# Optimization experiments

Hardware: AMD Instinct MI355X
Metric: run time of the kernel (lower is better)

The kernel has to match this reference:

```python
import jax, jax.numpy as jnp
import numpy as np

B, HEADS, N, D, K2 = 8, 8, 3136, 32, 9

def setup_inputs() -> dict:
    key = jax.random.key(0)
    k1, k2, k3, k4, k5 = jax.random.split(key, 5)
    return {
        "q_norm": jax.random.normal(k1, (B, HEADS, N, D), dtype=jnp.float32),
        "attn_local": jax.random.normal(k2, (B, HEADS, N, K2), dtype=jnp.float32),
        "v_local": jax.random.normal(k3, (B, HEADS, N, D, K2), dtype=jnp.float32),
        "learnable_tokens": jax.random.normal(k4, (HEADS, D, K2), dtype=jnp.float32),
        "learnable_bias": jax.random.normal(k5, (HEADS, N, K2), dtype=jnp.float32),
        "window_size": 3,
        "H": 56,
        "W": 56,
    }

def reference(q_norm, attn_local, v_local, learnable_tokens, learnable_bias, window_size, H, W):
    # attn = q_norm @ learnable_tokens + learnable_bias + attn_local  -> [B,h,N,k^2]
    attn = jnp.einsum('bhnd,hdk->bhnk', q_norm, learnable_tokens) + learnable_bias + attn_local
    # out = attn @ v_local^T over the window axis -> [B,h,N,d]
    return jnp.einsum('bhnk,bhndk->bhnd', attn, v_local)
```

## Files before the change

kernel.cpp:

```cpp
#include <hip/hip_runtime.h>

constexpr int Bc   = 8;
constexpr int Hh   = 8;
constexpr int Nn   = 3136;
constexpr int Dd   = 32;
constexpr int K2c  = 9;
constexpr int ROWS = Bc * Hh * Nn;
constexpr int ROWS_PER_BLOCK = 8;
constexpr int BLOCK = 256;

__global__ __launch_bounds__(BLOCK, 4)
void swattn_av_kernel(const float* __restrict__ q,
                      const float* __restrict__ attn_local,
                      const float* __restrict__ v,
                      const float* __restrict__ tok,
                      const float* __restrict__ bias,
                      float* __restrict__ out) {
    __shared__ float T_lds[Dd * K2c];
    __shared__ float q_lds[ROWS_PER_BLOCK][Dd + 1];
    __shared__ float attn_lds[ROWS_PER_BLOCK][K2c];

    const int tid  = threadIdx.x;
    const int base = blockIdx.x * ROWS_PER_BLOCK;
    const int h    = (base / Nn) % Hh;

    T_lds[tid < Dd * K2c ? tid : 0] = tok[h * Dd * K2c + (tid < Dd * K2c ? tid : 0)];
    if (tid < Dd * K2c - BLOCK)
        T_lds[BLOCK + tid] = tok[h * Dd * K2c + BLOCK + tid];
    {
        const int lrow = tid >> 5, d = tid & 31;
        q_lds[lrow][d] = q[(base + lrow) * Dd + d];
    }
    __syncthreads();

    if (tid < ROWS_PER_BLOCK * K2c) {
        const int lrow = tid / K2c;
        const int k    = tid - lrow * K2c;
        const int gr   = base + lrow;
        float s0 = 0.f, s1 = 0.f, s2 = 0.f, s3 = 0.f;
        #pragma unroll
        for (int d = 0; d < Dd; d += 4) {
            s0 += q_lds[lrow][d + 0] * T_lds[(d + 0) * K2c + k];
            s1 += q_lds[lrow][d + 1] * T_lds[(d + 1) * K2c + k];
            s2 += q_lds[lrow][d + 2] * T_lds[(d + 2) * K2c + k];
            s3 += q_lds[lrow][d + 3] * T_lds[(d + 3) * K2c + k];
        }
        const int bn = gr % (Hh * Nn);
        attn_lds[lrow][k] = ((s0 + s1) + (s2 + s3))
                          + attn_local[gr * K2c + k]
                          + bias[bn * K2c + k];
    }
    __syncthreads();

    {
        const int lrow = tid >> 5, d = tid & 31;
        const int gr   = base + lrow;
        const float* __restrict__ vr = v + (size_t)gr * (Dd * K2c) + d * K2c;
        float acc = 0.f;
        #pragma unroll
        for (int k = 0; k < K2c; ++k)
            acc += attn_lds[lrow][k] * vr[k];
        out[gr * Dd + d] = acc;
    }
}

extern "C" void kernel_launch(void* const* d_in, const int* in_sizes, int n_in,
                              void* d_out, int out_size, void* d_ws, size_t ws_size,
                              hipStream_t stream) {
    const float* q          = (const float*)d_in[0];
    const float* attn_local = (const float*)d_in[1];
    const float* v          = (const float*)d_in[2];
    const float* tok        = (const float*)d_in[3];
    const float* bias       = (const float*)d_in[4];
    float* out = (float*)d_out;

    const int grid = ROWS / ROWS_PER_BLOCK;
    swattn_av_kernel<<<grid, BLOCK, 0, stream>>>(q, attn_local, v, tok, bias, out);
}
```

Measured before the change: 343.8 us.

## Stage v tile through LDS with coalesced float4 loads and hoist global loads

Loads the block's contiguous v slab (8 rows x 288 floats) with coalesced float4 reads into shared memory, replacing strided per-thread reads of 9 floats at stride 36 bytes. All global loads (v, tok, q, attn_local, bias) are issued up front before the first barrier so their latency overlaps. Launch bounds are raised to request more resident blocks. In exchange the kernel uses about 9 KB more LDS per block, which may limit occupancy.

Result: no change. 347.4 us (+1.0%).

```diff
diff --git a/kernel.cpp b/kernel.cpp
--- a/kernel.cpp
+++ b/kernel.cpp
@@ -6,61 +6,86 @@
 constexpr int Dd   = 32;
 constexpr int K2c  = 9;
 constexpr int ROWS = Bc * Hh * Nn;
-constexpr int ROWS_PER_BLOCK = 8;
+constexpr int RPB  = 8;
 constexpr int BLOCK = 256;
+constexpr int VROW = Dd * K2c;
+constexpr int VBLK = RPB * VROW;
 
-__global__ __launch_bounds__(BLOCK, 4)
+__global__ __launch_bounds__(BLOCK, 8)
 void swattn_av_kernel(const float* __restrict__ q,
                       const float* __restrict__ attn_local,
                       const float* __restrict__ v,
                       const float* __restrict__ tok,
                       const float* __restrict__ bias,
                       float* __restrict__ out) {
-    __shared__ float T_lds[Dd * K2c];
-    __shared__ float q_lds[ROWS_PER_BLOCK][Dd + 1];
-    __shared__ float attn_lds[ROWS_PER_BLOCK][K2c];
+    __shared__ float T_lds[VROW];
+    __shared__ float q_lds[RPB][Dd + 1];
+    __shared__ float attn_lds[RPB][K2c];
+    __shared__ float v_lds[VBLK];
 
     const int tid  = threadIdx.x;
-    const int base = blockIdx.x * ROWS_PER_BLOCK;
+    const int base = blockIdx.x * RPB;
     const int h    = (base / Nn) % Hh;
+    const int lrow = tid >> 5, d = tid & 31;
 
-    T_lds[tid < Dd * K2c ? tid : 0] = tok[h * Dd * K2c + (tid < Dd * K2c ? tid : 0)];
-    if (tid < Dd * K2c - BLOCK)
-        T_lds[BLOCK + tid] = tok[h * Dd * K2c + BLOCK + tid];
-    {
-        const int lrow = tid >> 5, d = tid & 31;
-        q_lds[lrow][d] = q[(base + lrow) * Dd + d];
+    const float4* __restrict__ vsrc =
+        reinterpret_cast<const float4*>(v + (size_t)base * VROW);
+    float4* vdst = reinterpret_cast<float4*>(v_lds);
+    float4 vv0 = vsrc[tid];
+    float4 vv1 = vsrc[tid + 256];
+    float4 vv2 = make_float4(0.f, 0.f, 0.f, 0.f);
+    if (tid < VBLK / 4 - 512)
+        vv2 = vsrc[tid + 512];
+
+    float4 tt = make_float4(0.f, 0.f, 0.f, 0.f);
+    if (tid < VROW / 4)
+        tt = reinterpret_cast<const float4*>(tok + h * VROW)[tid];
+
+    const float qv = q[(base + lrow) * Dd + d];
+
+    float al = 0.f, bs = 0.f;
+    int arow = 0, ak = 0;
+    if (tid < RPB * K2c) {
+        arow = tid / K2c;
+        ak   = tid - arow * K2c;
+        const int gr = base + arow;
+        al = attn_local[gr * K2c + ak];
+        bs = bias[(gr % (Hh * Nn)) * K2c + ak];
     }
+
+    vdst[tid]       = vv0;
+    vdst[tid + 256] = vv1;
+    if (tid < VBLK / 4 - 512)
+        vdst[tid + 512] = vv2;
+    if (tid < VROW / 4)
+        reinterpret_cast<float4*>(T_lds)[tid] = tt;
+    q_lds[lrow][d] = qv;
     __syncthreads();
 
-    if (tid < ROWS_PER_BLOCK * K2c) {
-        const int lrow = tid / K2c;
-        const int k    = tid - lrow * K2c;
-        const int gr   = base + lrow;
+    if (tid < RPB * K2c) {
         float s0 = 0.f, s1 = 0.f, s2 = 0.f, s3 = 0.f;
         #pragma unroll
-        for (int d = 0; d < Dd; d += 4) {
-            s0 += q_lds[lrow][d + 0] * T_lds[(d + 0) * K2c + k];
-            s1 += q_lds[lrow][d + 1] * T_lds[(d + 1) * K2c + k];
-            s2 += q_lds[lrow][d + 2] * T_lds[(d + 2) * K2c + k];
-            s3 += q_lds[lrow][d + 3] * T_lds[(d + 3) * K2c + k];
+        for (int dd = 0; dd < Dd; dd += 4) {
+            s0 += q_lds[arow][dd + 0] * T_lds[(dd + 0) * K2c + ak];
+            s1 += q_lds[arow][dd + 1] * T_lds[(dd + 1) * K2c + ak];
+            s2 += q_lds[arow][dd + 2] * T_lds[(dd + 2) * K2c + ak];
+            s3 += q_lds[arow][dd + 3] * T_lds[(dd + 3) * K2c + ak];
         }
-        const int bn = gr % (Hh * Nn);
-        attn_lds[lrow][k] = ((s0 + s1) + (s2 + s3))
-                          + attn_local[gr * K2c + k]
-                          + bias[bn * K2c + k];
+        attn_lds[arow][ak] = ((s0 + s1) + (s2 + s3)) + al + bs;
     }
     __syncthreads();
 
     {
-        const int lrow = tid >> 5, d = tid & 31;
-        const int gr   = base + lrow;
-        const float* __restrict__ vr = v + (size_t)gr * (Dd * K2c) + d * K2c;
+        float a[K2c];
+        #pragma unroll
+        for (int k = 0; k < K2c; ++k)
+            a[k] = attn_lds[lrow][k];
+        const float* __restrict__ vr = v_lds + lrow * VROW + d * K2c;
         float acc = 0.f;
         #pragma unroll
         for (int k = 0; k < K2c; ++k)
-            acc += attn_lds[lrow][k] * vr[k];
-        out[gr * Dd + d] = acc;
+            acc += a[k] * vr[k];
+        out[(base + lrow) * Dd + d] = acc;
     }
 }
 
@@ -74,6 +99,6 @@
     const float* bias       = (const float*)d_in[4];
     float* out = (float*)d_out;
 
-    const int grid = ROWS / ROWS_PER_BLOCK;
+    const int grid = ROWS / RPB;
     swattn_av_kernel<<<grid, BLOCK, 0, stream>>>(q, attn_local, v, tok, bias, out);
 }
```

## Use persistent waves over contiguous row runs with register double-buffered prefetch

Applied to the files above, without the earlier changes.

Replaces the one-block-per-8-rows launch with a fixed grid in which each wavefront processes a contiguous run of rows, two rows per iteration, one per 32-lane half. The next row pair's v, q and attn/bias values are prefetched into registers while the current pair is computed. The q·tokens dot product is now done with butterfly shuffles instead of shared-memory staging and block barriers. This aims to hide global load latency and remove per-block sync and launch overhead. In exchange it raises register pressure and adds many shuffles per row, since the dot product is recomputed per k.

After: 370.1 us. 1.08x slower.

```diff
diff --git a/kernel.cpp b/kernel.cpp
--- a/kernel.cpp
+++ b/kernel.cpp
@@ -6,61 +6,77 @@
 constexpr int Dd   = 32;
 constexpr int K2c  = 9;
 constexpr int ROWS = Bc * Hh * Nn;
-constexpr int ROWS_PER_BLOCK = 8;
 constexpr int BLOCK = 256;
+constexpr int WPB   = BLOCK / 64;
+constexpr int GRID  = 1792;
+constexpr int NWAVE = GRID * WPB;
+constexpr int RUN   = ROWS / NWAVE;
+constexpr int ITERS = RUN / 2;
+static_assert(NWAVE * RUN == ROWS, "exact cover");
+static_assert(Nn % RUN == 0, "run never crosses a head boundary");
+constexpr int VROW = Dd * K2c;
 
-__global__ __launch_bounds__(BLOCK, 4)
+__global__ __launch_bounds__(BLOCK, 7)
 void swattn_av_kernel(const float* __restrict__ q,
                       const float* __restrict__ attn_local,
                       const float* __restrict__ v,
                       const float* __restrict__ tok,
                       const float* __restrict__ bias,
                       float* __restrict__ out) {
-    __shared__ float T_lds[Dd * K2c];
-    __shared__ float q_lds[ROWS_PER_BLOCK][Dd + 1];
-    __shared__ float attn_lds[ROWS_PER_BLOCK][K2c];
+    __shared__ float T_lds[VROW];
 
     const int tid  = threadIdx.x;
-    const int base = blockIdx.x * ROWS_PER_BLOCK;
-    const int h    = (base / Nn) % Hh;
+    const int lane = tid & 63;
+    const int wid  = tid >> 6;
+    const int W    = blockIdx.x * WPB + wid;
+    const int runBase = W * RUN;
+    const int h    = (runBase / Nn) & (Hh - 1);
+    const int half = lane >> 5;
+    const int d    = lane & 31;
+    const bool l9  = (d < K2c);
+    const int brem = runBase % (Hh * Nn) + half;
 
-    T_lds[tid < Dd * K2c ? tid : 0] = tok[h * Dd * K2c + (tid < Dd * K2c ? tid : 0)];
-    if (tid < Dd * K2c - BLOCK)
-        T_lds[BLOCK + tid] = tok[h * Dd * K2c + BLOCK + tid];
-    {
-        const int lrow = tid >> 5, d = tid & 31;
-        q_lds[lrow][d] = q[(base + lrow) * Dd + d];
-    }
+    if (tid < VROW / 4)
+        reinterpret_cast<float4*>(T_lds)[tid] =
+            reinterpret_cast<const float4*>(tok + h * VROW)[tid];
     __syncthreads();
 
-    if (tid < ROWS_PER_BLOCK * K2c) {
-        const int lrow = tid / K2c;
-        const int k    = tid - lrow * K2c;
-        const int gr   = base + lrow;
-        float s0 = 0.f, s1 = 0.f, s2 = 0.f, s3 = 0.f;
+    float vA[K2c], vB[K2c];
+    float qA = 0.f, qB = 0.f, aA = 0.f, aB = 0.f;
+
+    auto prefetch = [&](int i, float (&vr)[K2c], float& qr, float& ar) {
+        const int r0  = runBase + 2 * i;
+        const int row = r0 + half;
+        const float* __restrict__ vp = v + (size_t)row * VROW + d * K2c;
         #pragma unroll
-        for (int d = 0; d < Dd; d += 4) {
-            s0 += q_lds[lrow][d + 0] * T_lds[(d + 0) * K2c + k];
-            s1 += q_lds[lrow][d + 1] * T_lds[(d + 1) * K2c + k];
-            s2 += q_lds[lrow][d + 2] * T_lds[(d + 2) * K2c + k];
-            s3 += q_lds[lrow][d + 3] * T_lds[(d + 3) * K2c + k];
-        }
-        const int bn = gr % (Hh * Nn);
-        attn_lds[lrow][k] = ((s0 + s1) + (s2 + s3))
-                          + attn_local[gr * K2c + k]
-                          + bias[bn * K2c + k];
-    }
-    __syncthreads();
+        for (int k = 0; k < K2c; ++k) vr[k] = vp[k];
+        qr = q[r0 * Dd + lane];
+        if (l9)
+            ar = attn_local[row * K2c + d] + bias[(brem + 2 * i) * K2c + d];
+    };
 
-    {
-        const int lrow = tid >> 5, d = tid & 31;
-        const int gr   = base + lrow;
-        const float* __restrict__ vr = v + (size_t)gr * (Dd * K2c) + d * K2c;
+    auto compute = [&](int i, float (&vr)[K2c], float qr, float ar) {
         float acc = 0.f;
         #pragma unroll
-        for (int k = 0; k < K2c; ++k)
-            acc += attn_lds[lrow][k] * vr[k];
-        out[gr * Dd + d] = acc;
+        for (int k = 0; k < K2c; ++k) {
+            float p = qr * T_lds[d * K2c + k];
+            p += __shfl_xor(p, 1, 32);
+            p += __shfl_xor(p, 2, 32);
+            p += __shfl_xor(p, 4, 32);
+            p += __shfl_xor(p, 8, 32);
+            p += __shfl_xor(p, 16, 32);
+            acc += (p + __shfl(ar, k, 32)) * vr[k];
+        }
+        out[(runBase + 2 * i) * Dd + lane] = acc;
+    };
+
+    prefetch(0, vA, qA, aA);
+    #pragma unroll
+    for (int i = 0; i < ITERS; i += 2) {
+        prefetch(i + 1, vB, qB, aB);
+        compute(i, vA, qA, aA);
+        if (i + 2 < ITERS) prefetch(i + 2, vA, qA, aA);
+        compute(i + 1, vB, qB, aB);
     }
 }
 
@@ -74,6 +90,5 @@
     const float* bias       = (const float*)d_in[4];
     float* out = (float*)d_out;
 
-    const int grid = ROWS / ROWS_PER_BLOCK;
-    swattn_av_kernel<<<grid, BLOCK, 0, stream>>>(q, attn_local, v, tok, bias, out);
+    swattn_av_kernel<<<GRID, BLOCK, 0, stream>>>(q, attn_local, v, tok, bias, out);
 }
```

## Process 32 rows per block with float4 loads and early V prefetch

Applied to the files above, without the earlier changes.

Raises rows per block from 8 to 32. Each thread now handles 4 output dims of one row, loading its 36 contiguous V floats as nine float4 registers before the attention-score phase, so the dominant V traffic overlaps the score computation. Q, tokens and the output use vectorized float4 accesses, and attn_local and bias are loaded before the first barrier. The cost is higher register pressure from the prefetched V array, and the launch bound is raised to 6 waves per SIMD.

Result: no change. 348.1 us (+1.2%).

```diff
diff --git a/kernel.cpp b/kernel.cpp
--- a/kernel.cpp
+++ b/kernel.cpp
@@ -1,66 +1,94 @@
 #include <hip/hip_runtime.h>
 
-constexpr int Bc   = 8;
 constexpr int Hh   = 8;
 constexpr int Nn   = 3136;
 constexpr int Dd   = 32;
 constexpr int K2c  = 9;
-constexpr int ROWS = Bc * Hh * Nn;
-constexpr int ROWS_PER_BLOCK = 8;
+constexpr int ROWS = 8 * Hh * Nn;
+constexpr int RPB  = 32;
 constexpr int BLOCK = 256;
+constexpr int PAIRS = RPB * K2c;
+constexpr int VROW  = Dd * K2c;
+constexpr int GRID  = ROWS / RPB;
 
-__global__ __launch_bounds__(BLOCK, 4)
+__global__ __launch_bounds__(BLOCK, 6)
 void swattn_av_kernel(const float* __restrict__ q,
                       const float* __restrict__ attn_local,
                       const float* __restrict__ v,
                       const float* __restrict__ tok,
                       const float* __restrict__ bias,
                       float* __restrict__ out) {
-    __shared__ float T_lds[Dd * K2c];
-    __shared__ float q_lds[ROWS_PER_BLOCK][Dd + 1];
-    __shared__ float attn_lds[ROWS_PER_BLOCK][K2c];
+    __shared__ float T_lds[VROW];
+    __shared__ float q_lds[RPB][Dd + 1];
+    __shared__ float attn_lds[PAIRS];
 
     const int tid  = threadIdx.x;
-    const int base = blockIdx.x * ROWS_PER_BLOCK;
-    const int h    = (base / Nn) % Hh;
+    const int base = blockIdx.x * RPB;
+    const int h    = (base / Nn) & (Hh - 1);
+    const int brem = base % (Hh * Nn);
 
-    T_lds[tid < Dd * K2c ? tid : 0] = tok[h * Dd * K2c + (tid < Dd * K2c ? tid : 0)];
-    if (tid < Dd * K2c - BLOCK)
-        T_lds[BLOCK + tid] = tok[h * Dd * K2c + BLOCK + tid];
     {
-        const int lrow = tid >> 5, d = tid & 31;
-        q_lds[lrow][d] = q[(base + lrow) * Dd + d];
+        const float4 qv = reinterpret_cast<const float4*>(q + (size_t)base * Dd)[tid];
+        const int r = tid >> 3, c = (tid & 7) * 4;
+        q_lds[r][c + 0] = qv.x;
+        q_lds[r][c + 1] = qv.y;
+        q_lds[r][c + 2] = qv.z;
+        q_lds[r][c + 3] = qv.w;
     }
+    if (tid < VROW / 4)
+        reinterpret_cast<float4*>(T_lds)[tid] =
+            reinterpret_cast<const float4*>(tok + h * VROW)[tid];
+    const float a0 = attn_local[(size_t)base * K2c + tid] + bias[(size_t)brem * K2c + tid];
+    float a1 = 0.f;
+    if (tid < PAIRS - BLOCK)
+        a1 = attn_local[(size_t)base * K2c + BLOCK + tid]
+           + bias[(size_t)brem * K2c + BLOCK + tid];
     __syncthreads();
 
-    if (tid < ROWS_PER_BLOCK * K2c) {
-        const int lrow = tid / K2c;
-        const int k    = tid - lrow * K2c;
-        const int gr   = base + lrow;
-        float s0 = 0.f, s1 = 0.f, s2 = 0.f, s3 = 0.f;
+    const int row = tid >> 3;
+    const int d0  = (tid & 7) * 4;
+    float4 vf[9];
+    {
+        const float4* __restrict__ vp = reinterpret_cast<const float4*>(
+            v + (size_t)(base + row) * VROW + d0 * K2c);
         #pragma unroll
-        for (int d = 0; d < Dd; d += 4) {
-            s0 += q_lds[lrow][d + 0] * T_lds[(d + 0) * K2c + k];
-            s1 += q_lds[lrow][d + 1] * T_lds[(d + 1) * K2c + k];
-            s2 += q_lds[lrow][d + 2] * T_lds[(d + 2) * K2c + k];
-            s3 += q_lds[lrow][d + 3] * T_lds[(d + 3) * K2c + k];
-        }
-        const int bn = gr % (Hh * Nn);
-        attn_lds[lrow][k] = ((s0 + s1) + (s2 + s3))
-                          + attn_local[gr * K2c + k]
-                          + bias[bn * K2c + k];
+        for (int j = 0; j < 9; ++j) vf[j] = vp[j];
+    }
+
+    {
+        const int p  = tid, ar = p / K2c, ak = p - ar * K2c;
+        float s = 0.f;
+        #pragma unroll
+        for (int dd = 0; dd < Dd; ++dd)
+            s += q_lds[ar][dd] * T_lds[dd * K2c + ak];
+        attn_lds[p] = s + a0;
+    }
+    if (tid < PAIRS - BLOCK) {
+        const int p  = BLOCK + tid, ar = p / K2c, ak = p - ar * K2c;
+        float s = 0.f;
+        #pragma unroll
+        for (int dd = 0; dd < Dd; ++dd)
+            s += q_lds[ar][dd] * T_lds[dd * K2c + ak];
+        attn_lds[p] = s + a1;
     }
     __syncthreads();
 
     {
-        const int lrow = tid >> 5, d = tid & 31;
-        const int gr   = base + lrow;
-        const float* __restrict__ vr = v + (size_t)gr * (Dd * K2c) + d * K2c;
-        float acc = 0.f;
+        float af[K2c];
         #pragma unroll
         for (int k = 0; k < K2c; ++k)
-            acc += attn_lds[lrow][k] * vr[k];
-        out[gr * Dd + d] = acc;
+            af[k] = attn_lds[row * K2c + k];
+        float acc[4] = {0.f, 0.f, 0.f, 0.f};
+        #pragma unroll
+        for (int j = 0; j < 9; ++j) {
+            const float e0 = vf[j].x, e1 = vf[j].y, e2 = vf[j].z, e3 = vf[j].w;
+            acc[(4 * j + 0) / K2c] += af[(4 * j + 0) % K2c] * e0;
+            acc[(4 * j + 1) / K2c] += af[(4 * j + 1) % K2c] * e1;
+            acc[(4 * j + 2) / K2c] += af[(4 * j + 2) % K2c] * e2;
+            acc[(4 * j + 3) / K2c] += af[(4 * j + 3) % K2c] * e3;
+        }
+        float4 o; o.x = acc[0]; o.y = acc[1]; o.z = acc[2]; o.w = acc[3];
+        reinterpret_cast<float4*>(out + (size_t)(base + row) * Dd)[tid & 7] = o;
     }
 }
 
@@ -74,6 +102,5 @@
     const float* bias       = (const float*)d_in[4];
     float* out = (float*)d_out;
 
-    const int grid = ROWS / ROWS_PER_BLOCK;
-    swattn_av_kernel<<<grid, BLOCK, 0, stream>>>(q, attn_local, v, tok, bias, out);
+    swattn_av_kernel<<<GRID, BLOCK, 0, stream>>>(q, attn_local, v, tok, bias, out);
 }
```
